# Performance work log

Measured on AMD Instinct MI355X. Metric: run time of the kernel, lower is better.

The kernel has to match this reference:

```python
import jax, jax.numpy as jnp
import numpy as np

NEG_SLOPE = 0.01  # torch.nn.LeakyReLU default


def setup_inputs() -> dict:
    key = jax.random.key(0)
    ks = jax.random.split(key, 9)
    B, S, F1, F2, N, M, E, L = 2, 256, 512, 512, 20000, 2, 320000, 3
    x = jax.random.normal(ks[0], (B, S, F1), dtype=jnp.float32)
    nodes = jax.random.normal(ks[1], (N, M, F2), dtype=jnp.float32)
    edge_index = jax.random.randint(ks[2], (2, E), 0, N, dtype=jnp.int32)
    Wp = jax.random.normal(ks[3], (F1, F2), dtype=jnp.float32) * 0.02  # torch Linear weight [out,in]
    bp = jax.random.normal(ks[4], (F1,), dtype=jnp.float32) * 0.02
    gcn_W = jax.random.normal(ks[5], (L, S, S), dtype=jnp.float32) * 0.05  # stored as [in,out]
    gcn_b = jax.random.normal(ks[6], (L, S), dtype=jnp.float32) * 0.02
    w_bp = jax.random.normal(ks[7], (S,), dtype=jnp.float32) * 0.05
    b_bp = jax.random.normal(ks[8], (1,), dtype=jnp.float32) * 0.02
    return {"x": x, "nodes": nodes, "edge_index": edge_index, "Wp": Wp, "bp": bp,
            "gcn_W": gcn_W, "gcn_b": gcn_b, "w_bp": w_bp, "b_bp": b_bp}


def reference(x, nodes, edge_index, Wp, bp, gcn_W, gcn_b, w_bp, b_bp):
    # Eval mode: dropout layers are identity.
    N = nodes.shape[0]
    L = gcn_W.shape[0]
    proj = nodes @ Wp.T + bp                         # [N, M, F1]
    score = jnp.einsum('bsk,nmk->bsn', x, proj)      # sum over M and F1 -> [B, S, N]
    h = score.transpose(0, 2, 1)                     # beliefs [B, N, S]

    # GCN normalization with self-loops: D^{-1/2} (A + I) D^{-1/2}
    src, dst = edge_index[0], edge_index[1]
    loop = jnp.arange(N, dtype=edge_index.dtype)
    row = jnp.concatenate([src, loop])               # message sources
    col = jnp.concatenate([dst, loop])               # message targets
    deg = jnp.zeros((N,), dtype=h.dtype).at[col].add(1.0)
    dinv = deg ** -0.5                               # deg >= 1 due to self-loops
    norm = dinv[row] * dinv[col]                     # [E+N]

    for l in range(L):
        hw = h @ gcn_W[l]                            # [B, N, S]
        msg = hw[:, row, :] * norm[None, :, None]    # gather + scale
        agg = jnp.zeros_like(hw).at[:, col, :].add(msg) + gcn_b[l]
        h = jax.nn.leaky_relu(agg, NEG_SLOPE)

    # belief_projection: Linear(S, 1) then squeeze -> [B, N]
    return h @ w_bp + b_bp[0]
```

## Files before the change

### kernel.cpp

```cpp
#include <hip/hip_runtime.h>
#include <cstddef>
#include <cstdint>

#define NN 20000

typedef short frag16 __attribute__((ext_vector_type(8)));
typedef float f32x4 __attribute__((ext_vector_type(4)));

__device__ inline unsigned short f32_to_bf16(float f) {
    uint32_t u = __float_as_uint(f);
    u += 0x7FFFu + ((u >> 16) & 1u);
    return (unsigned short)(u >> 16);
}

__device__ inline float4 dec4(uint2 v) {
    float4 r;
    r.x = __uint_as_float(v.x << 16);
    r.y = __uint_as_float(v.x & 0xffff0000u);
    r.z = __uint_as_float(v.y << 16);
    r.w = __uint_as_float(v.y & 0xffff0000u);
    return r;
}

__global__ __launch_bounds__(256) void prep(
    const float* __restrict__ nodes, const float* __restrict__ x,
    const float* __restrict__ gcn_W, const float* __restrict__ bp,
    const int* __restrict__ src, const int* __restrict__ dst,
    unsigned short* __restrict__ nsum16, unsigned short* __restrict__ WT,
    float* __restrict__ Tf, float* __restrict__ cvec,
    int* __restrict__ cnt, int* __restrict__ csr, int E)
{
    __shared__ __align__(16) char shmem[8704];
    const int blk = blockIdx.x, tid = threadIdx.x;

    if (blk < 64) {
        float* As = (float*)shmem;
        float* Bs = As + 1024;
        int b = blk >> 5, rem = blk & 31;
        int s0 = (rem >> 3) * 64, f0 = (rem & 7) * 64;
        const float* W1 = gcn_W;
        const float* xb = x + (size_t)b * 256 * 512;
        int kk = tid >> 4, c4 = (tid & 15) << 2;
        int tm = tid >> 4, tn = tid & 15;
        float acc[4][4] = {};
        for (int k0 = 0; k0 < 256; k0 += 16) {
            float4 av = *(const float4*)(W1 + (size_t)(k0 + kk) * 256 + s0 + c4);
            float4 bv = *(const float4*)(xb + (size_t)(k0 + kk) * 512 + f0 + c4);
            __syncthreads();
            *(float4*)&As[kk * 64 + c4] = av;
            *(float4*)&Bs[kk * 64 + c4] = bv;
            __syncthreads();
            #pragma unroll
            for (int k = 0; k < 16; ++k) {
                float a[4], bb[4];
                *(float4*)a  = *(const float4*)&As[k * 64 + (tm << 2)];
                *(float4*)bb = *(const float4*)&Bs[k * 64 + (tn << 2)];
                #pragma unroll
                for (int i = 0; i < 4; ++i)
                    #pragma unroll
                    for (int j = 0; j < 4; ++j) acc[i][j] += a[i] * bb[j];
            }
        }
        #pragma unroll
        for (int i = 0; i < 4; ++i) {
            int row = b * 256 + s0 + (tm << 2) + i;
            *(float4*)(Tf + (size_t)row * 512 + f0 + (tn << 2)) =
                make_float4(acc[i][0], acc[i][1], acc[i][2], acc[i][3]);
        }
    } else if (blk < 2576) {
        int g = (blk - 64) * 256 + tid;
        int n = g >> 5, c = (g & 31) << 4;
        uint4 o0, o1;
        if (n < NN) {
            const float* r0 = nodes + (size_t)n * 1024 + c;
            const float* r1 = r0 + 512;
            float4 a0 = *(const float4*)(r0 + 0),  a1 = *(const float4*)(r0 + 4);
            float4 a2 = *(const float4*)(r0 + 8),  a3 = *(const float4*)(r0 + 12);
            float4 b0 = *(const float4*)(r1 + 0),  b1 = *(const float4*)(r1 + 4);
            float4 b2 = *(const float4*)(r1 + 8),  b3 = *(const float4*)(r1 + 12);
            o0.x = ((uint32_t)f32_to_bf16(a0.y + b0.y) << 16) | f32_to_bf16(a0.x + b0.x);
            o0.y = ((uint32_t)f32_to_bf16(a0.w + b0.w) << 16) | f32_to_bf16(a0.z + b0.z);
            o0.z = ((uint32_t)f32_to_bf16(a1.y + b1.y) << 16) | f32_to_bf16(a1.x + b1.x);
            o0.w = ((uint32_t)f32_to_bf16(a1.w + b1.w) << 16) | f32_to_bf16(a1.z + b1.z);
            o1.x = ((uint32_t)f32_to_bf16(a2.y + b2.y) << 16) | f32_to_bf16(a2.x + b2.x);
            o1.y = ((uint32_t)f32_to_bf16(a2.w + b2.w) << 16) | f32_to_bf16(a2.z + b2.z);
            o1.z = ((uint32_t)f32_to_bf16(a3.y + b3.y) << 16) | f32_to_bf16(a3.x + b3.x);
            o1.w = ((uint32_t)f32_to_bf16(a3.w + b3.w) << 16) | f32_to_bf16(a3.z + b3.z);
        } else {
            o0 = make_uint4(0, 0, 0, 0); o1 = o0;
        }
        *(uint4*)(nsum16 + (size_t)n * 512 + c) = o0;
        *(uint4*)(nsum16 + (size_t)n * 512 + c + 8) = o1;
    } else if (blk < 2608) {
        unsigned short (*tsh)[68] = (unsigned short(*)[68])shmem;
        int t = blk - 2576;
        int l = t >> 4, rem = t & 15;
        int c0 = (rem & 3) * 64, r0 = (rem >> 2) * 64;
        const float* inp = gcn_W + (size_t)(l + 1) * 65536;
        unsigned short* outp = WT + (size_t)l * 65536;
        int tx = tid & 15, ty = tid >> 4;
        #pragma unroll
        for (int rr = 0; rr < 4; ++rr) {
            int r = ty * 4 + rr;
            float4 v = *(const float4*)(inp + (size_t)(r0 + r) * 256 + c0 + tx * 4);
            tsh[tx * 4 + 0][r] = f32_to_bf16(v.x);
            tsh[tx * 4 + 1][r] = f32_to_bf16(v.y);
            tsh[tx * 4 + 2][r] = f32_to_bf16(v.z);
            tsh[tx * 4 + 3][r] = f32_to_bf16(v.w);
        }
        __syncthreads();
        #pragma unroll
        for (int cc = 0; cc < 4; ++cc) {
            int c = ty * 4 + cc;
            ushort4 o = *(ushort4*)&tsh[c][tx * 4];
            *(ushort4*)(outp + (size_t)(c0 + c) * 256 + r0 + tx * 4) = o;
        }
    } else if (blk < 2736) {
        int row = (blk - 2608) * 4 + (tid >> 6);
        int lane = tid & 63;
        const float* xr = x + (size_t)row * 512;
        float s = 0.f;
        #pragma unroll
        for (int k = 0; k < 512; k += 64) s += xr[k + lane] * bp[k + lane];
        #pragma unroll
        for (int off = 32; off; off >>= 1) s += __shfl_down(s, off);
        if (lane == 0) cvec[row] = 2.0f * s;
    } else {
        int e = (blk - 2736) * 256 + tid;
        if (e < E) {
            int d = dst[e];
            int pos = atomicAdd(&cnt[d], 1);
            if (pos < 64) csr[(d << 6) + pos] = src[e];
        }
    }
}

__global__ __launch_bounds__(256) void mid(
    const float* __restrict__ Tf, const float* __restrict__ Wp,
    const float* __restrict__ gcn_W, const float* __restrict__ cvec,
    unsigned short* __restrict__ Ub, float* __restrict__ cb2)
{
    const int blk = blockIdx.x, tid = threadIdx.x;
    if (blk >= 64) {
        int idx = (blk - 64) * 256 + tid;
        int b = idx >> 8, s = idx & 255;
        float sum = 0.f;
        for (int sp = 0; sp < 256; ++sp)
            sum += gcn_W[(size_t)sp * 256 + s] * cvec[b * 256 + sp];
        cb2[idx] = sum;
        return;
    }
    __shared__ float As[16][68];
    __shared__ float Bs[16][64];
    int bm = (blk >> 3) * 64, bn = (blk & 7) * 64;
    int arow = tid >> 2, acol = (tid & 3) << 2;
    int brow = tid >> 4, bcol = (tid & 15) << 2;
    int tm = tid >> 4, tn = tid & 15;
    float acc[4][4] = {};
    for (int k0 = 0; k0 < 512; k0 += 16) {
        float4 av = *(const float4*)(Tf + (size_t)(bm + arow) * 512 + k0 + acol);
        float4 bv = *(const float4*)(Wp + (size_t)(k0 + brow) * 512 + bn + bcol);
        __syncthreads();
        As[acol + 0][arow] = av.x; As[acol + 1][arow] = av.y;
        As[acol + 2][arow] = av.z; As[acol + 3][arow] = av.w;
        *(float4*)&Bs[brow][bcol] = bv;
        __syncthreads();
        #pragma unroll
        for (int k = 0; k < 16; ++k) {
            float a[4], b[4];
            *(float4*)a = *(const float4*)&As[k][tm << 2];
            *(float4*)b = *(const float4*)&Bs[k][tn << 2];
            #pragma unroll
            for (int i = 0; i < 4; ++i)
                #pragma unroll
                for (int j = 0; j < 4; ++j) acc[i][j] += a[i] * b[j];
        }
    }
    #pragma unroll
    for (int i = 0; i < 4; ++i) {
        int row = bm + (tm << 2) + i;
        ushort4 o;
        o.x = f32_to_bf16(acc[i][0]); o.y = f32_to_bf16(acc[i][1]);
        o.z = f32_to_bf16(acc[i][2]); o.w = f32_to_bf16(acc[i][3]);
        *(ushort4*)(Ub + (size_t)row * 512 + bn + (tn << 2)) = o;
    }
}

__global__ __launch_bounds__(256) void mgemm(
    const unsigned short* __restrict__ A, const unsigned short* __restrict__ BT,
    int K, int N, int mode,
    const float* __restrict__ cb2, const int* __restrict__ cnt,
    unsigned short* __restrict__ C)
{
    __shared__ __align__(16) unsigned short As[128 * 32];
    __shared__ __align__(16) unsigned short Bs[128 * 32];
    const int bm = blockIdx.y * 128, bn = blockIdx.x * 128;
    const int tid = threadIdx.x;
    const int lane = tid & 63, w = tid >> 6;
    const int wm = (w >> 1) << 6, wn = (w & 1) << 6;
    const int r = lane & 15, q = lane >> 4;

    f32x4 acc[4][4] = {};

    for (int k0 = 0; k0 < K; k0 += 32) {
        __syncthreads();
        #pragma unroll
        for (int t = 0; t < 2; ++t) {
            int c = t * 256 + w * 64 + lane;
            int row = c >> 2, col = (c & 3) << 3;
            __builtin_amdgcn_global_load_lds(
                (const __attribute__((address_space(1))) void*)(A + (size_t)(bm + row) * K + k0 + col),
                (__attribute__((address_space(3))) void*)(As + (size_t)(t * 256 + w * 64) * 8),
                16, 0, 0);
            __builtin_amdgcn_global_load_lds(
                (const __attribute__((address_space(1))) void*)(BT + (size_t)(bn + row) * K + k0 + col),
                (__attribute__((address_space(3))) void*)(Bs + (size_t)(t * 256 + w * 64) * 8),
                16, 0, 0);
        }
        __syncthreads();
        frag16 af[4], bf[4];
        #pragma unroll
        for (int i = 0; i < 4; ++i)
            af[i] = *(const frag16*)(As + ((wm + i * 16 + r) << 5) + (q << 3));
        #pragma unroll
        for (int j = 0; j < 4; ++j)
            bf[j] = *(const frag16*)(Bs + ((wn + j * 16 + r) << 5) + (q << 3));
        #pragma unroll
        for (int i = 0; i < 4; ++i)
            #pragma unroll
            for (int j = 0; j < 4; ++j)
                acc[i][j] = __builtin_amdgcn_mfma_f32_16x16x32_bf16(af[i], bf[j], acc[i][j], 0, 0, 0);
    }

    #pragma unroll
    for (int i = 0; i < 4; ++i) {
        #pragma unroll
        for (int rg = 0; rg < 4; ++rg) {
            int m = bm + wm + i * 16 + (q << 2) + rg;
            float sc;
            int b2 = 0, node = m;
            if (mode == 1) {
                int nc = m > NN - 1 ? NN - 1 : m;
                sc = rsqrtf((float)cnt[nc] + 1.0f);
            } else {
                b2 = m >= NN;
                node = m - b2 * NN;
                int nc = node > NN - 1 ? NN - 1 : node;
                sc = rsqrtf((float)cnt[nc] + 1.0f);
                if (node > 20095) node = 20095;
            }
            #pragma unroll
            for (int j = 0; j < 4; ++j) {
                int n = bn + wn + j * 16 + r;
                if (mode == 1) {
                    float v = (acc[i][j][rg] + cb2[n]) * sc;
                    C[(size_t)m * 512 + n] = f32_to_bf16(v);
                } else {
                    float v = acc[i][j][rg] * sc;
                    C[(size_t)node * 512 + (b2 << 8) + n] = f32_to_bf16(v);
                }
            }
        }
    }
}

__global__ __launch_bounds__(256) void aggregate_s(
    const unsigned short* __restrict__ hw, const int* __restrict__ cnt,
    const int* __restrict__ csr, const float* __restrict__ bias,
    unsigned short* __restrict__ hout,
    const float* __restrict__ w_bp, const float* __restrict__ b_bp,
    float* __restrict__ out)
{
    int n = blockIdx.x * 4 + (threadIdx.x >> 6);
    int b = blockIdx.y;
    int lane = threadIdx.x & 63;
    const unsigned short* rowp = hw + (b << 8) + (lane << 2);

    float4 acc = dec4(*(const uint2*)(rowp + (size_t)n * 512));
    int deg = cnt[n]; if (deg > 64) deg = 64;
    const int* cp = csr + (n << 6);
    int e = 0;
    for (; e + 8 <= deg; e += 8) {
        int4 c0 = *(const int4*)(cp + e);
        int4 c1 = *(const int4*)(cp + e + 4);
        uint2 u0 = *(const uint2*)(rowp + (size_t)c0.x * 512);
        uint2 u1 = *(const uint2*)(rowp + (size_t)c0.y * 512);
        uint2 u2 = *(const uint2*)(rowp + (size_t)c0.z * 512);
        uint2 u3 = *(const uint2*)(rowp + (size_t)c0.w * 512);
        uint2 u4 = *(const uint2*)(rowp + (size_t)c1.x * 512);
        uint2 u5 = *(const uint2*)(rowp + (size_t)c1.y * 512);
        uint2 u6 = *(const uint2*)(rowp + (size_t)c1.z * 512);
        uint2 u7 = *(const uint2*)(rowp + (size_t)c1.w * 512);
        float4 f0 = dec4(u0), f1 = dec4(u1), f2 = dec4(u2), f3 = dec4(u3);
        float4 f4 = dec4(u4), f5 = dec4(u5), f6 = dec4(u6), f7 = dec4(u7);
        acc.x += ((f0.x + f1.x) + (f2.x + f3.x)) + ((f4.x + f5.x) + (f6.x + f7.x));
        acc.y += ((f0.y + f1.y) + (f2.y + f3.y)) + ((f4.y + f5.y) + (f6.y + f7.y));
        acc.z += ((f0.z + f1.z) + (f2.z + f3.z)) + ((f4.z + f5.z) + (f6.z + f7.z));
        acc.w += ((f0.w + f1.w) + (f2.w + f3.w)) + ((f4.w + f5.w) + (f6.w + f7.w));
    }
    for (; e < deg; ++e) {
        float4 f = dec4(*(const uint2*)(rowp + (size_t)cp[e] * 512));
        acc.x += f.x; acc.y += f.y; acc.z += f.z; acc.w += f.w;
    }

    float dn = rsqrtf((float)deg + 1.0f);
    int s = lane << 2;
    float4 bl = *(const float4*)(bias + s);
    float4 v;
    v.x = fmaf(dn, acc.x, bl.x); v.y = fmaf(dn, acc.y, bl.y);
    v.z = fmaf(dn, acc.z, bl.z); v.w = fmaf(dn, acc.w, bl.w);
    v.x = v.x > 0.f ? v.x : 0.01f * v.x;
    v.y = v.y > 0.f ? v.y : 0.01f * v.y;
    v.z = v.z > 0.f ? v.z : 0.01f * v.z;
    v.w = v.w > 0.f ? v.w : 0.01f * v.w;

    if (out) {
        float4 w4 = *(const float4*)(w_bp + s);
        float sum = v.x * w4.x + v.y * w4.y + v.z * w4.z + v.w * w4.w;
        #pragma unroll
        for (int off = 32; off; off >>= 1) sum += __shfl_xor(sum, off);
        if (lane == 0) out[b * NN + n] = sum + b_bp[0];
    } else {
        uint2 o;
        o.x = ((uint32_t)f32_to_bf16(v.y) << 16) | f32_to_bf16(v.x);
        o.y = ((uint32_t)f32_to_bf16(v.w) << 16) | f32_to_bf16(v.z);
        *(uint2*)(hout + ((size_t)(b * NN + n)) * 256 + s) = o;
    }
}

extern "C" void kernel_launch(void* const* d_in, const int* in_sizes, int n_in,
                              void* d_out, int out_size, void* d_ws, size_t ws_size,
                              hipStream_t stream) {
    const float* x     = (const float*)d_in[0];
    const float* nodes = (const float*)d_in[1];
    const int*   eidx  = (const int*)d_in[2];
    const float* Wp    = (const float*)d_in[3];
    const float* bp    = (const float*)d_in[4];
    const float* gcn_W = (const float*)d_in[5];
    const float* gcn_b = (const float*)d_in[6];
    const float* w_bp  = (const float*)d_in[7];
    const float* b_bp  = (const float*)d_in[8];
    const int E = in_sizes[2] / 2;

    char* w = (char*)d_ws;
    auto alloc = [&](size_t bytes) { char* p = w; w += (bytes + 255) & ~(size_t)255; return p; };
    unsigned short* nsum16 = (unsigned short*)alloc((size_t)20096 * 512 * 2);
    unsigned short* hw16   = (unsigned short*)alloc((size_t)20096 * 512 * 2);
    unsigned short* hA     = (unsigned short*)alloc((size_t)40192 * 256 * 2);
    unsigned short* hB     = (unsigned short*)alloc((size_t)40192 * 256 * 2);
    float* Tf  = (float*)alloc((size_t)512 * 512 * 4);
    unsigned short* Ub = (unsigned short*)alloc((size_t)512 * 512 * 2);
    unsigned short* WT = (unsigned short*)alloc((size_t)2 * 256 * 256 * 2);
    float* cvec = (float*)alloc(512 * 4);
    float* cb2  = (float*)alloc(512 * 4);
    int*   cnt  = (int*)alloc((size_t)NN * 4);
    int*   csr  = (int*)alloc((size_t)NN * 64 * 4);

    hipMemsetAsync(cnt, 0, (size_t)NN * 4, stream);

    const int cntBlks = (E + 255) / 256;
    prep<<<2736 + cntBlks, 256, 0, stream>>>(nodes, x, gcn_W, bp, eidx, eidx + E,
                                             nsum16, WT, Tf, cvec, cnt, csr, E);
    mid<<<66, 256, 0, stream>>>(Tf, Wp, gcn_W, cvec, Ub, cb2);

    mgemm<<<dim3(4, 157), 256, 0, stream>>>(nsum16, Ub, 512, 512, 1, cb2, cnt, hw16);

    aggregate_s<<<dim3(5000, 2), 256, 0, stream>>>(hw16, cnt, csr, gcn_b + 0, hA,
                                                   w_bp, b_bp, nullptr);
    mgemm<<<dim3(2, 313), 256, 0, stream>>>(hA, WT, 256, 256, 2, nullptr, cnt, hw16);
    aggregate_s<<<dim3(5000, 2), 256, 0, stream>>>(hw16, cnt, csr, gcn_b + 256, hB,
                                                   w_bp, b_bp, nullptr);
    mgemm<<<dim3(2, 313), 256, 0, stream>>>(hB, WT + 65536, 256, 256, 2, nullptr, cnt, hw16);
    aggregate_s<<<dim3(5000, 2), 256, 0, stream>>>(hw16, cnt, csr, gcn_b + 512, nullptr,
                                                   w_bp, b_bp, (float*)d_out);
}
```

Baseline: 388.5 us.

## Split GCN aggregation across channel chunks and schedule edge counting first

The aggregation kernel now gives each wave a 64-channel slice of one node, so eight blocks cover the node's 512 channels across both batches. Before, one wave covered all 256 channels of a single batch using 4-channel vector loads. The final projection is now summed across chunks with atomicAdd into a zero-initialised output. In prep, the edge-counting/CSR blocks move to the front of the grid so the atomics start early. The change aims at more parallelism and latency hiding on the gathers, but it trades this for scalar 2-byte loads, eight times more index reads, and atomic output accumulation.

```diff
diff --git a/kernel.cpp b/kernel.cpp
--- a/kernel.cpp
+++ b/kernel.cpp
@@ -13,13 +13,8 @@
     return (unsigned short)(u >> 16);
 }
 
-__device__ inline float4 dec4(uint2 v) {
-    float4 r;
-    r.x = __uint_as_float(v.x << 16);
-    r.y = __uint_as_float(v.x & 0xffff0000u);
-    r.z = __uint_as_float(v.y << 16);
-    r.w = __uint_as_float(v.y & 0xffff0000u);
-    return r;
+__device__ inline float bf1(unsigned short h) {
+    return __uint_as_float((uint32_t)h << 16);
 }
 
 __global__ __launch_bounds__(256) void prep(
@@ -32,11 +27,20 @@
 {
     __shared__ __align__(16) char shmem[8704];
     const int blk = blockIdx.x, tid = threadIdx.x;
-
-    if (blk < 64) {
+    const int eb = (E + 255) >> 8;
+
+    if (blk < eb) {
+        int e = blk * 256 + tid;
+        if (e < E) {
+            int d = dst[e];
+            int pos = atomicAdd(&cnt[d], 1);
+            if (pos < 64) csr[(d << 6) + pos] = src[e];
+        }
+    } else if (blk < eb + 64) {
         float* As = (float*)shmem;
         float* Bs = As + 1024;
-        int b = blk >> 5, rem = blk & 31;
+        int t = blk - eb;
+        int b = t >> 5, rem = t & 31;
         int s0 = (rem >> 3) * 64, f0 = (rem & 7) * 64;
         const float* W1 = gcn_W;
         const float* xb = x + (size_t)b * 256 * 512;
@@ -67,8 +71,8 @@
             *(float4*)(Tf + (size_t)row * 512 + f0 + (tn << 2)) =
                 make_float4(acc[i][0], acc[i][1], acc[i][2], acc[i][3]);
         }
-    } else if (blk < 2576) {
-        int g = (blk - 64) * 256 + tid;
+    } else if (blk < eb + 64 + 2512) {
+        int g = (blk - eb - 64) * 256 + tid;
         int n = g >> 5, c = (g & 31) << 4;
         uint4 o0, o1;
         if (n < NN) {
@@ -91,9 +95,9 @@
         }
         *(uint4*)(nsum16 + (size_t)n * 512 + c) = o0;
         *(uint4*)(nsum16 + (size_t)n * 512 + c + 8) = o1;
-    } else if (blk < 2608) {
+    } else if (blk < eb + 64 + 2512 + 32) {
         unsigned short (*tsh)[68] = (unsigned short(*)[68])shmem;
-        int t = blk - 2576;
+        int t = blk - eb - 64 - 2512;
         int l = t >> 4, rem = t & 15;
         int c0 = (rem & 3) * 64, r0 = (rem >> 2) * 64;
         const float* inp = gcn_W + (size_t)(l + 1) * 65536;
@@ -115,8 +119,8 @@
             ushort4 o = *(ushort4*)&tsh[c][tx * 4];
             *(ushort4*)(outp + (size_t)(c0 + c) * 256 + r0 + tx * 4) = o;
         }
-    } else if (blk < 2736) {
-        int row = (blk - 2608) * 4 + (tid >> 6);
+    } else {
+        int row = (blk - eb - 64 - 2512 - 32) * 4 + (tid >> 6);
         int lane = tid & 63;
         const float* xr = x + (size_t)row * 512;
         float s = 0.f;
@@ -125,13 +129,6 @@
         #pragma unroll
         for (int off = 32; off; off >>= 1) s += __shfl_down(s, off);
         if (lane == 0) cvec[row] = 2.0f * s;
-    } else {
-        int e = (blk - 2736) * 256 + tid;
-        if (e < E) {
-            int d = dst[e];
-            int pos = atomicAdd(&cnt[d], 1);
-            if (pos < 64) csr[(d << 6) + pos] = src[e];
-        }
     }
 }
 
@@ -264,67 +261,66 @@
     }
 }
 
-__global__ __launch_bounds__(256) void aggregate_s(
+__global__ __launch_bounds__(256) void aggregate_c(
     const unsigned short* __restrict__ hw, const int* __restrict__ cnt,
     const int* __restrict__ csr, const float* __restrict__ bias,
     unsigned short* __restrict__ hout,
     const float* __restrict__ w_bp, const float* __restrict__ b_bp,
     float* __restrict__ out)
 {
-    int n = blockIdx.x * 4 + (threadIdx.x >> 6);
-    int b = blockIdx.y;
+    int blk = blockIdx.x;
+    int c = blk & 7;
+    int n = (blk >> 3) * 4 + (threadIdx.x >> 6);
     int lane = threadIdx.x & 63;
-    const unsigned short* rowp = hw + (b << 8) + (lane << 2);
-
-    float4 acc = dec4(*(const uint2*)(rowp + (size_t)n * 512));
+    int ch = (c << 6) + lane;
+    const unsigned short* colp = hw + ch;
+
+    float acc = bf1(colp[(size_t)n * 512]);
     int deg = cnt[n]; if (deg > 64) deg = 64;
     const int* cp = csr + (n << 6);
     int e = 0;
     for (; e + 8 <= deg; e += 8) {
         int4 c0 = *(const int4*)(cp + e);
         int4 c1 = *(const int4*)(cp + e + 4);
-        uint2 u0 = *(const uint2*)(rowp + (size_t)c0.x * 512);
-        uint2 u1 = *(const uint2*)(rowp + (size_t)c0.y * 512);
-        uint2 u2 = *(const uint2*)(rowp + (size_t)c0.z * 512);
-        uint2 u3 = *(const uint2*)(rowp + (size_t)c0.w * 512);
-        uint2 u4 = *(const uint2*)(rowp + (size_t)c1.x * 512);
-        uint2 u5 = *(const uint2*)(rowp + (size_t)c1.y * 512);
-        uint2 u6 = *(const uint2*)(rowp + (size_t)c1.z * 512);
-        uint2 u7 = *(const uint2*)(rowp + (size_t)c1.w * 512);
-        float4 f0 = dec4(u0), f1 = dec4(u1), f2 = dec4(u2), f3 = dec4(u3);
-        float4 f4 = dec4(u4), f5 = dec4(u5), f6 = dec4(u6), f7 = dec4(u7);
-        acc.x += ((f0.x + f1.x) + (f2.x + f3.x)) + ((f4.x + f5.x) + (f6.x + f7.x));
-        acc.y += ((f0.y + f1.y) + (f2.y + f3.y)) + ((f4.y + f5.y) + (f6.y + f7.y));
-        acc.z += ((f0.z + f1.z) + (f2.z + f3.z)) + ((f4.z + f5.z) + (f6.z + f7.z));
-        acc.w += ((f0.w + f1.w) + (f2.w + f3.w)) + ((f4.w + f5.w) + (f6.w + f7.w));
-    }
-    for (; e < deg; ++e) {
-        float4 f = dec4(*(const uint2*)(rowp + (size_t)cp[e] * 512));
-        acc.x += f.x; acc.y += f.y; acc.z += f.z; acc.w += f.w;
-    }
+        unsigned short u0 = colp[(size_t)c0.x * 512];
+        unsigned short u1 = colp[(size_t)c0.y * 512];
+        unsigned short u2 = colp[(size_t)c0.z * 512];
+        unsigned short u3 = colp[(size_t)c0.w * 512];
+        unsigned short u4 = colp[(size_t)c1.x * 512];
+        unsigned short u5 = colp[(size_t)c1.y * 512];
+        unsigned short u6 = colp[(size_t)c1.z * 512];
+        unsigned short u7 = colp[(size_t)c1.w * 512];
+        acc += ((bf1(u0) + bf1(u1)) + (bf1(u2) + bf1(u3)))
+             + ((bf1(u4) + bf1(u5)) + (bf1(u6) + bf1(u7)));
+    }
+    if (e + 4 <= deg) {
+        int4 c0 = *(const int4*)(cp + e);
+        unsigned short u0 = colp[(size_t)c0.x * 512];
+        unsigned short u1 = colp[(size_t)c0.y * 512];
+        unsigned short u2 = colp[(size_t)c0.z * 512];
+        unsigned short u3 = colp[(size_t)c0.w * 512];
+        acc += (bf1(u0) + bf1(u1)) + (bf1(u2) + bf1(u3));
+        e += 4;
+    }
+    for (; e < deg; ++e)
+        acc += bf1(colp[(size_t)cp[e] * 512]);
 
     float dn = rsqrtf((float)deg + 1.0f);
-    int s = lane << 2;
-    float4 bl = *(const float4*)(bias + s);
-    float4 v;
-    v.x = fmaf(dn, acc.x, bl.x); v.y = fmaf(dn, acc.y, bl.y);
-    v.z = fmaf(dn, acc.z, bl.z); v.w = fmaf(dn, acc.w, bl.w);
-    v.x = v.x > 0.f ? v.x : 0.01f * v.x;
-    v.y = v.y > 0.f ? v.y : 0.01f * v.y;
-    v.z = v.z > 0.f ? v.z : 0.01f * v.z;
-    v.w = v.w > 0.f ? v.w : 0.01f * v.w;
+    int s = ch & 255;
+    int b = c >> 2;
+    float v = fmaf(dn, acc, bias[s]);
+    v = v > 0.f ? v : 0.01f * v;
 
     if (out) {
-        float4 w4 = *(const float4*)(w_bp + s);
-        float sum = v.x * w4.x + v.y * w4.y + v.z * w4.z + v.w * w4.w;
-        #pragma unroll
-        for (int off = 32; off; off >>= 1) sum += __shfl_xor(sum, off);
-        if (lane == 0) out[b * NN + n] = sum + b_bp[0];
+        float p = v * w_bp[s];
+        #pragma unroll
+        for (int off = 32; off; off >>= 1) p += __shfl_xor(p, off);
+        if (lane == 0) {
+            if ((c & 3) == 0) p += b_bp[0];
+            atomicAdd(&out[b * NN + n], p);
+        }
     } else {
-        uint2 o;
-        o.x = ((uint32_t)f32_to_bf16(v.y) << 16) | f32_to_bf16(v.x);
-        o.y = ((uint32_t)f32_to_bf16(v.w) << 16) | f32_to_bf16(v.z);
-        *(uint2*)(hout + ((size_t)(b * NN + n)) * 256 + s) = o;
+        hout[((size_t)(b * NN + n)) * 256 + s] = f32_to_bf16(v);
     }
 }
 
@@ -357,20 +353,21 @@
     int*   csr  = (int*)alloc((size_t)NN * 64 * 4);
 
     hipMemsetAsync(cnt, 0, (size_t)NN * 4, stream);
+    hipMemsetAsync(d_out, 0, (size_t)out_size * 4, stream);
 
     const int cntBlks = (E + 255) / 256;
-    prep<<<2736 + cntBlks, 256, 0, stream>>>(nodes, x, gcn_W, bp, eidx, eidx + E,
-                                             nsum16, WT, Tf, cvec, cnt, csr, E);
+    prep<<<cntBlks + 64 + 2512 + 32 + 128, 256, 0, stream>>>(
+        nodes, x, gcn_W, bp, eidx, eidx + E, nsum16, WT, Tf, cvec, cnt, csr, E);
     mid<<<66, 256, 0, stream>>>(Tf, Wp, gcn_W, cvec, Ub, cb2);
 
     mgemm<<<dim3(4, 157), 256, 0, stream>>>(nsum16, Ub, 512, 512, 1, cb2, cnt, hw16);
 
-    aggregate_s<<<dim3(5000, 2), 256, 0, stream>>>(hw16, cnt, csr, gcn_b + 0, hA,
-                                                   w_bp, b_bp, nullptr);
+    aggregate_c<<<40000, 256, 0, stream>>>(hw16, cnt, csr, gcn_b + 0, hA,
+                                           w_bp, b_bp, nullptr);
     mgemm<<<dim3(2, 313), 256, 0, stream>>>(hA, WT, 256, 256, 2, nullptr, cnt, hw16);
-    aggregate_s<<<dim3(5000, 2), 256, 0, stream>>>(hw16, cnt, csr, gcn_b + 256, hB,
-                                                   w_bp, b_bp, nullptr);
+    aggregate_c<<<40000, 256, 0, stream>>>(hw16, cnt, csr, gcn_b + 256, hB,
+                                           w_bp, b_bp, nullptr);
     mgemm<<<dim3(2, 313), 256, 0, stream>>>(hB, WT + 65536, 256, 256, 2, nullptr, cnt, hw16);
-    aggregate_s<<<dim3(5000, 2), 256, 0, stream>>>(hw16, cnt, csr, gcn_b + 512, nullptr,
-                                                   w_bp, b_bp, (float*)d_out);
-}
+    aggregate_c<<<40000, 256, 0, stream>>>(hw16, cnt, csr, gcn_b + 512, nullptr,
+                                           w_bp, b_bp, (float*)d_out);
+}
```

After: 494.7 us. +27.3%, slower.
